# Kernel tuning notes

Hardware: AMD Instinct MI355X
Metric: run time of the kernel (lower is better)

## Reference

```python
import jax, jax.numpy as jnp
import numpy as np

B, NN, BBX, CLS, LAT = 8192, 64, 6, 16, 128
IN = LAT + NN + CLS  # 208
NT = B * NN          # total nodes in batched graph
NE = 4_194_304       # random edges (avg degree 8)


def setup_inputs() -> dict:
    key = jax.random.key(0)
    ks = jax.random.split(key, 16)
    p = lambda i, sh: (jax.random.normal(ks[i], sh, dtype=jnp.float32) * 0.05)
    return {
        "embedding": jax.random.normal(ks[0], (B, IN), dtype=jnp.float32),
        "E": jax.random.randint(ks[1], (2, NE), 0, NT, dtype=jnp.int32),
        "refine_iter": 2,
        "W1": p(2, (IN, 128)), "b1": p(3, (128,)),
        "W2": p(4, (128, 128)), "b2": p(5, (128,)),
        "Wbbx": p(6, (128, NN * BBX)), "bbbx": p(7, (NN * BBX,)),
        "Wlbl": p(8, (128, NN)), "blbl": p(9, (NN,)),
        "Wedge": p(10, (128, NN * NN)), "bedge": p(11, (NN * NN,)),
        "Wcls": p(12, (128, CLS)), "bcls": p(13, (CLS,)),
        "Wg": p(14, (BBX, BBX)), "bg": p(15, (BBX,)),
    }


def _gcn(h, src, dst, Wg, bg):
    # PyG GCNConv with add_self_loops=True, bias: D^-1/2 (A+I) D^-1/2 (h W) + b
    deg = jax.ops.segment_sum(jnp.ones(src.shape, h.dtype), dst, num_segments=NT)
    dinv = jax.lax.rsqrt(deg)  # deg >= 1 thanks to self-loops
    norm = dinv[src] * dinv[dst]
    m = h @ Wg  # [NT, BBX]
    out = jax.ops.segment_sum(m[src] * norm[:, None], dst, num_segments=NT)
    return out + bg


def reference(embedding, E, refine_iter, W1, b1, W2, b2, Wbbx, bbbx,
              Wlbl, blbl, Wedge, bedge, Wcls, bcls, Wg, bg):
    sig = jax.nn.sigmoid
    x = sig(embedding @ W1 + b1)
    x = sig(x @ W2 + b2)
    x = sig(x @ W2 + b2)  # dense2 applied twice (shared weights), as in source
    x_bbx = sig(x @ Wbbx + bbbx).reshape(B, NN, BBX)
    x_lbl = sig(x @ Wlbl + blbl).reshape(B, NN, 1)
    x_edge = sig(x @ Wedge + bedge).reshape(B, NN, NN)
    class_pred = jax.nn.softmax(x @ Wcls + bcls, axis=-1)

    loops = jnp.arange(NT, dtype=E.dtype)
    src = jnp.concatenate([E[0], loops])
    dst = jnp.concatenate([E[1], loops])

    x_bbx_refined = x_bbx
    for _ in range(int(refine_iter)):
        x_masked = x_bbx_refined * x_lbl  # labels=None -> mask with x_lbl
        flat = x_masked.reshape(NT, BBX)
        corr = jax.nn.sigmoid(_gcn(flat, src, dst, Wg, bg))
        # NOTE: source adds correction to the MASKED features (faithful)
        x_bbx_refined = (flat + corr).reshape(B, NN, BBX)
    return (x_bbx, x_lbl, x_edge, class_pred, x_bbx_refined)
```

## Files before the change

### kernel.cpp

```cpp
#include <hip/hip_runtime.h>
#include <hip/hip_bf16.h>
#include <math.h>

#define B_      8192
#define IN_     208
#define INP_    224
#define H_      128
#define NN_     64
#define BBX_    6
#define CLS_    16
#define NT_     (B_*NN_)
#define NE_     4194304
#define NB_     256
#define BSH_    11
#define CH_     4096
#define CAP_    18432

typedef __attribute__((ext_vector_type(8))) short short8v;
typedef __attribute__((ext_vector_type(4))) float f32x4;
typedef __attribute__((ext_vector_type(2))) float f32x2;

__device__ __forceinline__ float sigmoidf_(float v){ return 1.0f/(1.0f+__expf(-v)); }
__device__ __forceinline__ unsigned f2bf_(float f){
  unsigned u = __float_as_uint(f);
  return (u + 0x7FFFu + ((u >> 16) & 1u)) >> 16;
}

#if defined(__has_builtin)
# if __has_builtin(__builtin_amdgcn_cvt_pk_fp8_f32) && __has_builtin(__builtin_amdgcn_cvt_pk_f32_fp8)
#  define HW_FP8 1
# endif
#endif
#ifndef HW_FP8
# define HW_FP8 0
#endif

#if !HW_FP8
__device__ __forceinline__ unsigned enc1_(float v){
  unsigned u = __float_as_uint(v);
  unsigned s = (u >> 31) << 7;
  unsigned a = u & 0x7FFFFFFFu;
  unsigned r8;
  if (a < 0x3D000000u) {
    int q = (int)rintf(__uint_as_float(a) * 512.0f);
    r8 = (unsigned)q;
  } else {
    unsigned r = a + 0x7FFFFu + ((a >> 20) & 1u);
    int eb = (int)(r >> 23) - 120;
    r8 = (eb > 15) ? 0x7Eu : (unsigned)((eb << 3) | ((r >> 20) & 7u));
  }
  return s | r8;
}
__device__ __forceinline__ float dec1_(unsigned b){
  unsigned m = b & 7u, e = (b >> 3) & 0xFu;
  float mag = e ? __uint_as_float(((e + 120u) << 23) | (m << 20))
               : (float)m * 0.001953125f;
  return (b & 0x80u) ? -mag : mag;
}
#endif

__device__ __forceinline__ uint2 enc6_(const float mm[6]){
  uint2 o;
#if HW_FP8
  int w0 = __builtin_amdgcn_cvt_pk_fp8_f32(mm[0], mm[1], 0, false);
  w0     = __builtin_amdgcn_cvt_pk_fp8_f32(mm[2], mm[3], w0, true);
  int w1 = __builtin_amdgcn_cvt_pk_fp8_f32(mm[4], mm[5], 0, false);
  o.x = (unsigned)w0; o.y = (unsigned)w1;
#else
  o.x = enc1_(mm[0]) | (enc1_(mm[1])<<8) | (enc1_(mm[2])<<16) | (enc1_(mm[3])<<24);
  o.y = enc1_(mm[4]) | (enc1_(mm[5])<<8);
#endif
  return o;
}
__device__ __forceinline__ void dec6_(uint2 w, float v[6]){
#if HW_FP8
  f32x2 a = __builtin_amdgcn_cvt_pk_f32_fp8(w.x, false);
  f32x2 b = __builtin_amdgcn_cvt_pk_f32_fp8(w.x, true);
  f32x2 c = __builtin_amdgcn_cvt_pk_f32_fp8(w.y, false);
  v[0]=a[0]; v[1]=a[1]; v[2]=b[0]; v[3]=b[1]; v[4]=c[0]; v[5]=c[1];
#else
  v[0]=dec1_(w.x & 255u); v[1]=dec1_((w.x>>8)&255u);
  v[2]=dec1_((w.x>>16)&255u); v[3]=dec1_(w.x>>24);
  v[4]=dec1_(w.y & 255u); v[5]=dec1_((w.y>>8)&255u);
#endif
}

__global__ __launch_bounds__(256) void gemm_bias_act(
    const float* __restrict__ A, const float* __restrict__ W,
    const float* __restrict__ bias, float* __restrict__ C,
    int M, int N, int K, int act)
{
  __shared__ float As[16][64];
  __shared__ float Bs[16][64];
  const int tid = threadIdx.x;
  const int bm = blockIdx.y * 64;
  const int bn = blockIdx.x * 64;
  const int tx = tid & 15;
  const int ty = tid >> 4;
  const int arow = tid >> 2;
  const int acol = (tid & 3) << 2;
  const int brow = tid >> 4;
  const int bcol = (tid & 15) << 2;

  float acc[4][4] = {};

  for (int k0 = 0; k0 < K; k0 += 16) {
    float4 av = *reinterpret_cast<const float4*>(A + (size_t)(bm + arow) * K + k0 + acol);
    float4 bv = *reinterpret_cast<const float4*>(W + (size_t)(k0 + brow) * N + bn + bcol);
    __syncthreads();
    As[acol+0][arow] = av.x; As[acol+1][arow] = av.y;
    As[acol+2][arow] = av.z; As[acol+3][arow] = av.w;
    *reinterpret_cast<float4*>(&Bs[brow][bcol]) = bv;
    __syncthreads();
    #pragma unroll
    for (int k = 0; k < 16; ++k) {
      float4 a = *reinterpret_cast<const float4*>(&As[k][ty << 2]);
      float4 b = *reinterpret_cast<const float4*>(&Bs[k][tx << 2]);
      float ar[4] = {a.x, a.y, a.z, a.w};
      float br[4] = {b.x, b.y, b.z, b.w};
      #pragma unroll
      for (int i = 0; i < 4; ++i)
        #pragma unroll
        for (int j = 0; j < 4; ++j)
          acc[i][j] = fmaf(ar[i], br[j], acc[i][j]);
    }
  }

  #pragma unroll
  for (int i = 0; i < 4; ++i) {
    const int row = bm + (ty << 2) + i;
    float4 o;
    float* op = &o.x;
    #pragma unroll
    for (int j = 0; j < 4; ++j) {
      float v = acc[i][j] + bias[bn + (tx << 2) + j];
      op[j] = act ? sigmoidf_(v) : v;
    }
    *reinterpret_cast<float4*>(C + (size_t)row * N + bn + (tx << 2)) = o;
  }
}

__global__ __launch_bounds__(256) void prep_k(
    const float* __restrict__ We, unsigned short* __restrict__ WtE,
    const float* __restrict__ Wb, unsigned short* __restrict__ WtB,
    const float* __restrict__ W2, unsigned short* __restrict__ Wt2,
    const float* __restrict__ W1, unsigned short* __restrict__ W1t)
{
  __shared__ unsigned short tile[64][136];
  const int t = threadIdx.x;
  if (blockIdx.x >= 72) {
    const int i = (blockIdx.x - 72) * 256 + t;
    if (i < H_ * INP_) {
      const int n = i / INP_, k = i % INP_;
      W1t[i] = (k < IN_) ? (unsigned short)f2bf_(W1[(size_t)k * H_ + n]) : 0;
    }
    return;
  }
  const float* W; unsigned short* Wt; int N, n0;
  if (blockIdx.x < 64)      { W = We; Wt = WtE; N = 4096; n0 = blockIdx.x * 64; }
  else if (blockIdx.x < 70) { W = Wb; Wt = WtB; N = 384;  n0 = (blockIdx.x-64) * 64; }
  else                      { W = W2; Wt = Wt2; N = 128;  n0 = (blockIdx.x-70) * 64; }
  const int kk = t >> 6;
  const int nn = t & 63;
  for (int k0 = 0; k0 < 128; k0 += 4)
    tile[nn][k0 + kk] = (unsigned short)f2bf_(W[(size_t)(k0 + kk) * N + n0 + nn]);
  __syncthreads();
  const int rr = t >> 2, c0 = (t & 3) * 32;
  ushort4* dst = reinterpret_cast<ushort4*>(Wt + (size_t)(n0 + rr) * 128 + c0);
  #pragma unroll
  for (int q = 0; q < 8; ++q) {
    ushort4 o;
    o.x = tile[rr][c0 + q*4 + 0]; o.y = tile[rr][c0 + q*4 + 1];
    o.z = tile[rr][c0 + q*4 + 2]; o.w = tile[rr][c0 + q*4 + 3];
    dst[q] = o;
  }
}

__global__ __launch_bounds__(256) void fused_trunk_k(
    const float* __restrict__ emb,
    const unsigned short* __restrict__ W1t,
    const float* __restrict__ b1,
    const unsigned short* __restrict__ W2t,
    const float* __restrict__ b2,
    unsigned short* __restrict__ Xb, float* __restrict__ xB)
{
  __shared__ unsigned short s[128][136];
  const int tid  = threadIdx.x;
  const int wave = tid >> 6, lane = tid & 63;
  const int wm = wave >> 1, wn = wave & 1;
  const int r = lane & 15, g = lane >> 4;
  const int colB0 = wn * 64;
  const int growA = blockIdx.x * 128 + wm * 64;

  f32x4 acc[4][4];
  short8v a[4], b[4];

  #pragma unroll
  for (int i = 0; i < 4; ++i)
    #pragma unroll
    for (int j = 0; j < 4; ++j)
      acc[i][j] = (f32x4){0.f, 0.f, 0.f, 0.f};

  for (int ks = 0; ks < INP_/32; ++ks) {
    const int koff = ks * 32 + g * 8;
    #pragma unroll
    for (int i = 0; i < 4; ++i) {
      if (koff < IN_) {
        const float* src = emb + (size_t)(growA + i*16 + r) * IN_ + koff;
        float4 v0 = *reinterpret_cast<const float4*>(src);
        float4 v1 = *reinterpret_cast<const float4*>(src + 4);
        a[i][0]=(short)f2bf_(v0.x); a[i][1]=(short)f2bf_(v0.y);
        a[i][2]=(short)f2bf_(v0.z); a[i][3]=(short)f2bf_(v0.w);
        a[i][4]=(short)f2bf_(v1.x); a[i][5]=(short)f2bf_(v1.y);
        a[i][6]=(short)f2bf_(v1.z); a[i][7]=(short)f2bf_(v1.w);
      } else {
        a[i] = (short8v){0,0,0,0,0,0,0,0};
      }
    }
    #pragma unroll
    for (int j = 0; j < 4; ++j)
      b[j] = *reinterpret_cast<const short8v*>(W1t + (size_t)(colB0 + j*16 + r) * INP_ + koff);
    #pragma unroll
    for (int i = 0; i < 4; ++i)
      #pragma unroll
      for (int j = 0; j < 4; ++j)
        acc[i][j] = __builtin_amdgcn_mfma_f32_16x16x32_bf16(a[i], b[j], acc[i][j], 0, 0, 0);
  }
  #pragma unroll
  for (int j = 0; j < 4; ++j) {
    const int col = colB0 + j*16 + r;
    const float bc = b1[col];
    #pragma unroll
    for (int i = 0; i < 4; ++i)
      #pragma unroll
      for (int q = 0; q < 4; ++q)
        s[wm*64 + i*16 + g*4 + q][col] = (unsigned short)f2bf_(sigmoidf_(acc[i][j][q] + bc));
  }
  __syncthreads();

  for (int layer = 0; layer < 2; ++layer) {
    #pragma unroll
    for (int i = 0; i < 4; ++i)
      #pragma unroll
      for (int j = 0; j < 4; ++j)
        acc[i][j] = (f32x4){0.f, 0.f, 0.f, 0.f};

    #pragma unroll
    for (int ks = 0; ks < 4; ++ks) {
      const int koff = ks * 32 + g * 8;
      #pragma unroll
      for (int i = 0; i < 4; ++i)
        a[i] = *reinterpret_cast<const short8v*>(&s[wm*64 + i*16 + r][koff]);
      #pragma unroll
      for (int j = 0; j < 4; ++j)
        b[j] = *reinterpret_cast<const short8v*>(W2t + (size_t)(colB0 + j*16 + r) * H_ + koff);
      #pragma unroll
      for (int i = 0; i < 4; ++i)
        #pragma unroll
        for (int j = 0; j < 4; ++j)
          acc[i][j] = __builtin_amdgcn_mfma_f32_16x16x32_bf16(a[i], b[j], acc[i][j], 0, 0, 0);
    }
    __syncthreads();

    if (layer == 0) {
      #pragma unroll
      for (int j = 0; j < 4; ++j) {
        const int col = colB0 + j*16 + r;
        const float bc = b2[col];
        #pragma unroll
        for (int i = 0; i < 4; ++i)
          #pragma unroll
          for (int q = 0; q < 4; ++q)
            s[wm*64 + i*16 + g*4 + q][col] = (unsigned short)f2bf_(sigmoidf_(acc[i][j][q] + bc));
      }
      __syncthreads();
    } else {
      #pragma unroll
      for (int j = 0; j < 4; ++j) {
        const int col = colB0 + j*16 + r;
        const float bc = b2[col];
        #pragma unroll
        for (int i = 0; i < 4; ++i) {
          const int grow = blockIdx.x*128 + wm*64 + i*16 + g*4;
          #pragma unroll
          for (int q = 0; q < 4; ++q) {
            const float v = sigmoidf_(acc[i][j][q] + bc);
            Xb[(size_t)(grow + q) * H_ + col] = (unsigned short)f2bf_(v);
            xB[(size_t)(grow + q) * H_ + col] = v;
          }
        }
      }
    }
  }
}

__global__ __launch_bounds__(256) void gemm_mfma_head(
    const unsigned short* __restrict__ Xb,
    const unsigned short* __restrict__ Wt,
    const float* __restrict__ bias, float* __restrict__ C, int N)
{
  const int tid  = threadIdx.x;
  const int wave = tid >> 6, lane = tid & 63;
  const int wm = wave >> 1, wn = wave & 1;
  const int r = lane & 15, g = lane >> 4;
  const int rowA0 = blockIdx.y * 128 + wm * 64;
  const int colB0 = blockIdx.x * 128 + wn * 64;

  f32x4 acc[4][4];
  #pragma unroll
  for (int i = 0; i < 4; ++i)
    #pragma unroll
    for (int j = 0; j < 4; ++j)
      acc[i][j] = (f32x4){0.f, 0.f, 0.f, 0.f};

  #pragma unroll
  for (int ks = 0; ks < 4; ++ks) {
    const int koff = ks * 32 + g * 8;
    short8v a[4], b[4];
    #pragma unroll
    for (int i = 0; i < 4; ++i)
      a[i] = *reinterpret_cast<const short8v*>(Xb + (size_t)(rowA0 + i*16 + r) * 128 + koff);
    #pragma unroll
    for (int j = 0; j < 4; ++j)
      b[j] = *reinterpret_cast<const short8v*>(Wt + (size_t)(colB0 + j*16 + r) * 128 + koff);
    #pragma unroll
    for (int i = 0; i < 4; ++i)
      #pragma unroll
      for (int j = 0; j < 4; ++j)
        acc[i][j] = __builtin_amdgcn_mfma_f32_16x16x32_bf16(a[i], b[j], acc[i][j], 0, 0, 0);
  }

  #pragma unroll
  for (int j = 0; j < 4; ++j) {
    const int col = colB0 + j*16 + r;
    const float bc = bias[col];
    #pragma unroll
    for (int i = 0; i < 4; ++i) {
      const int row0 = rowA0 + i*16 + g*4;
      #pragma unroll
      for (int q = 0; q < 4; ++q)
        C[(size_t)(row0 + q) * N + col] = sigmoidf_(acc[i][j][q] + bc);
    }
  }
}

__global__ __launch_bounds__(64) void cls_softmax_k(
    const float* __restrict__ X, const float* __restrict__ Wc,
    const float* __restrict__ bc, float* __restrict__ out)
{
  const int tid = threadIdx.x;
  const int r = blockIdx.x * 4 + (tid >> 4);
  const int c = tid & 15;
  const float* xr = X + (size_t)r * H_;
  float acc = bc[c];
  #pragma unroll 8
  for (int k = 0; k < H_; ++k) acc = fmaf(xr[k], Wc[k * CLS_ + c], acc);
  float mx = acc;
  for (int off = 8; off; off >>= 1) mx = fmaxf(mx, __shfl_xor(mx, off, 16));
  float e = __expf(acc - mx);
  float s = e;
  for (int off = 8; off; off >>= 1) s += __shfl_xor(s, off, 16);
  out[(size_t)r * CLS_ + c] = e / s;
}

__global__ __launch_bounds__(256) void binA_k(const int* __restrict__ E,
                                              int* __restrict__ gcnt,
                                              unsigned* __restrict__ binned) {
  __shared__ unsigned stage[CH_];
  __shared__ unsigned char stb[CH_];
  __shared__ int hist[NB_], lbase[NB_], gbase[NB_];
  const int t = threadIdx.x;
  const int e0 = blockIdx.x * CH_;

  hist[t] = 0;
  __syncthreads();

  unsigned pk[CH_/256];
  int rb[CH_/256];
  #pragma unroll
  for (int i = 0; i < CH_/256; ++i) {
    const int e = e0 + i * 256 + t;
    const int s = E[e];
    const unsigned d = (unsigned)E[NE_ + e];
    const int b = d >> BSH_;
    pk[i] = (unsigned)s | ((d & 2047u) << 19);
    rb[i] = atomicAdd(&hist[b], 1) | (b << 20);
  }
  __syncthreads();

  const int v = hist[t];
  lbase[t] = v; __syncthreads();
  #pragma unroll
  for (int off = 1; off < NB_; off <<= 1) {
    int x = (t >= off) ? lbase[t - off] : 0;
    __syncthreads();
    lbase[t] += x;
    __syncthreads();
  }
  const int excl = lbase[t] - v;
  __syncthreads();
  lbase[t] = excl;
  gbase[t] = t * CAP_ + atomicAdd(&gcnt[t], v);
  __syncthreads();

  #pragma unroll
  for (int i = 0; i < CH_/256; ++i) {
    const int b = rb[i] >> 20;
    const int pos = lbase[b] + (rb[i] & 0xFFFFF);
    stage[pos] = pk[i];
    stb[pos] = (unsigned char)b;
  }
  __syncthreads();

  for (int i = t; i < CH_; i += 256) {
    const int b = stb[i];
    const int tgt = gbase[b] + (i - lbase[b]);
    if (tgt < (b + 1) * CAP_)
      binned[tgt] = stage[i];
  }
}

__global__ __launch_bounds__(1024) void csr_k(const int* __restrict__ gcnt,
                                              const unsigned* __restrict__ binned,
                                              int* __restrict__ rowptr, int* __restrict__ cnt_g,
                                              float* __restrict__ dinv, int* __restrict__ csr_src) {
  __shared__ int cnt[2048];
  __shared__ int sd[1024];
  const int t = threadIdx.x, b = blockIdx.x;
  const int beg = b * CAP_;
  const int end = beg + min(gcnt[b], CAP_);

  cnt[t] = 0; cnt[t + 1024] = 0;
  __syncthreads();
  for (int i = beg + t; i < end; i += 1024)
    atomicAdd(&cnt[binned[i] >> 19], 1);
  __syncthreads();

  const int c0 = cnt[2 * t], c1 = cnt[2 * t + 1];
  const int s = c0 + c1;
  sd[t] = s; __syncthreads();
  #pragma unroll
  for (int off = 1; off < 1024; off <<= 1) {
    int x = (t >= off) ? sd[t - off] : 0;
    __syncthreads();
    sd[t] += x;
    __syncthreads();
  }
  const int excl = sd[t] - s;

  const int node0 = b * 2048 + 2 * t;
  rowptr[node0]     = beg + excl;
  rowptr[node0 + 1] = beg + excl + c0;
  cnt_g[node0]      = c0;
  cnt_g[node0 + 1]  = c1;
  dinv[node0]       = rsqrtf(1.0f + (float)c0);
  dinv[node0 + 1]   = rsqrtf(1.0f + (float)c1);
  __syncthreads();
  cnt[2 * t] = excl;
  cnt[2 * t + 1] = excl + c0;
  __syncthreads();

  for (int i = beg + t; i < end; i += 1024) {
    const unsigned pk = binned[i];
    const int dl = pk >> 19;
    const int slot = atomicAdd(&cnt[dl], 1);
    csr_src[beg + slot] = (int)(pk & 0x7FFFFu);
  }
}

__global__ __launch_bounds__(256) void gcn_pre_k(
    const float* __restrict__ refined, const float* __restrict__ lbl,
    const float* __restrict__ Wg, const float* __restrict__ dinv,
    uint2* __restrict__ ms8)
{
  int i = blockIdx.x * 256 + threadIdx.x;
  if (i >= NT_) return;
  float l = lbl[i];
  float di = dinv[i];
  float f[6];
  #pragma unroll
  for (int j = 0; j < 6; ++j) f[j] = refined[(size_t)i * 6 + j] * l;
  float mm[6];
  #pragma unroll
  for (int j = 0; j < 6; ++j) {
    float acc = 0.f;
    #pragma unroll
    for (int k = 0; k < 6; ++k) acc = fmaf(f[k], Wg[k * 6 + j], acc);
    mm[j] = acc * di;
  }
  ms8[i] = enc6_(mm);
}

template<int WRITE_MS>
__global__ __launch_bounds__(256) void gcn_gather_k(
    const float* __restrict__ rin, float* __restrict__ rout,
    const float* __restrict__ lbl,
    const uint2* __restrict__ ms8_in, uint2* __restrict__ ms8_out,
    const float* __restrict__ dinv,
    const int* __restrict__ rowptr, const int* __restrict__ cnt,
    const int* __restrict__ csr_src, const float* __restrict__ bg,
    const float* __restrict__ Wg)
{
  int i = blockIdx.x * 256 + threadIdx.x;
  if (i >= NT_) return;
  const float di = dinv[i];
  const float l  = lbl[i];
  const int beg = rowptr[i];
  const int kend = beg + cnt[i];

  float acc[6];
  dec6_(ms8_in[i], acc);

  int k = beg;
  for (; k + 7 < kend; k += 8) {
    int s_[8];
    uint2 w_[8];
    #pragma unroll
    for (int u = 0; u < 8; ++u) s_[u] = csr_src[k + u];
    #pragma unroll
    for (int u = 0; u < 8; ++u) w_[u] = ms8_in[s_[u]];
    #pragma unroll
    for (int u = 0; u < 8; ++u) {
      float v[6];
      dec6_(w_[u], v);
      #pragma unroll
      for (int j = 0; j < 6; ++j) acc[j] += v[j];
    }
  }
  for (; k + 3 < kend; k += 4) {
    const int s0 = csr_src[k],   s1 = csr_src[k+1];
    const int s2 = csr_src[k+2], s3 = csr_src[k+3];
    const uint2 w0 = ms8_in[s0], w1 = ms8_in[s1];
    const uint2 w2 = ms8_in[s2], w3 = ms8_in[s3];
    float v0[6], v1[6], v2[6], v3[6];
    dec6_(w0, v0); dec6_(w1, v1); dec6_(w2, v2); dec6_(w3, v3);
    #pragma unroll
    for (int j = 0; j < 6; ++j) acc[j] += (v0[j] + v1[j]) + (v2[j] + v3[j]);
  }
  for (; k < kend; ++k) {
    float v[6];
    dec6_(ms8_in[csr_src[k]], v);
    #pragma unroll
    for (int j = 0; j < 6; ++j) acc[j] += v[j];
  }

  float nr[6];
  #pragma unroll
  for (int j = 0; j < 6; ++j) {
    const float flat = rin[(size_t)i * 6 + j] * l;
    nr[j] = flat + sigmoidf_(di * acc[j] + bg[j]);
    rout[(size_t)i * 6 + j] = nr[j];
  }

  if (WRITE_MS) {
    float f[6], mm[6];
    #pragma unroll
    for (int j = 0; j < 6; ++j) f[j] = nr[j] * l;
    #pragma unroll
    for (int j = 0; j < 6; ++j) {
      float a = 0.f;
      #pragma unroll
      for (int kk = 0; kk < 6; ++kk) a = fmaf(f[kk], Wg[kk * 6 + j], a);
      mm[j] = a * di;
    }
    ms8_out[i] = enc6_(mm);
  }
}

extern "C" void kernel_launch(void* const* d_in, const int* in_sizes, int n_in,
                              void* d_out, int out_size, void* d_ws, size_t ws_size,
                              hipStream_t stream)
{
  const float* emb   = (const float*)d_in[0];
  const int*   E     = (const int*)  d_in[1];
  const float* W1    = (const float*)d_in[3];
  const float* b1    = (const float*)d_in[4];
  const float* W2    = (const float*)d_in[5];
  const float* b2    = (const float*)d_in[6];
  const float* Wbbx  = (const float*)d_in[7];
  const float* bbbx  = (const float*)d_in[8];
  const float* Wlbl  = (const float*)d_in[9];
  const float* blbl  = (const float*)d_in[10];
  const float* Wedge = (const float*)d_in[11];
  const float* bedge = (const float*)d_in[12];
  const float* Wcls  = (const float*)d_in[13];
  const float* bcls  = (const float*)d_in[14];
  const float* Wg    = (const float*)d_in[15];
  const float* bg    = (const float*)d_in[16];

  float* out    = (float*)d_out;
  float* o_bbx  = out;
  float* o_lbl  = out + 3145728;
  float* o_edge = out + 3670016;
  float* o_cls  = out + 37224448;
  float* o_ref  = out + 37355520;

  char* wsb = (char*)d_ws;
  float* xB      = (float*)wsb;
  float* dinv    = xB + (size_t)B_ * H_;
  int*   cnt_g   = (int*)(dinv + NT_);
  int*   rowptr  = cnt_g + NT_;
  int*   csr_src = rowptr + NT_;
  char*  U       = (char*)(csr_src + (size_t)NB_ * CAP_);
  unsigned*       binned = (unsigned*)U;
  unsigned short* Xb   = (unsigned short*)U;
  unsigned short* W1t  = Xb  + (size_t)B_ * H_;
  unsigned short* W2t  = W1t + (size_t)H_ * INP_;
  unsigned short* Wt_e = W2t + (size_t)H_ * H_;
  unsigned short* Wt_b = Wt_e + (size_t)4096 * H_;
  uint2*          ms8A = (uint2*)(Wt_b + (size_t)384 * H_);
  uint2*          ms8B = ms8A + NT_;
  int*            gcnt = (int*)(U + (size_t)NB_ * CAP_ * 4);

  hipMemsetAsync(gcnt, 0, NB_ * sizeof(int), stream);
  binA_k<<<NE_/CH_, 256, 0, stream>>>(E, gcnt, binned);
  csr_k <<<NB_, 1024, 0, stream>>>(gcnt, binned, rowptr, cnt_g, dinv, csr_src);

  prep_k<<<72 + (H_*INP_+255)/256, 256, 0, stream>>>(Wedge, Wt_e, Wbbx, Wt_b, W2, W2t, W1, W1t);

  fused_trunk_k<<<B_/128, 256, 0, stream>>>(emb, W1t, b1, W2t, b2, Xb, xB);

  gemm_mfma_head<<<dim3(4096/128, B_/128), 256, 0, stream>>>(Xb, Wt_e, bedge, o_edge, 4096);
  gemm_mfma_head<<<dim3(384/128,  B_/128), 256, 0, stream>>>(Xb, Wt_b, bbbx,  o_bbx,  384);
  gemm_bias_act<<<dim3(64/64, B_/64), 256, 0, stream>>>(xB, Wlbl, blbl, o_lbl, B_, 64, 128, 1);
  cls_softmax_k<<<B_/4, 64, 0, stream>>>(xB, Wcls, bcls, o_cls);

  gcn_pre_k<<<NT_/256, 256, 0, stream>>>(o_bbx, o_lbl, Wg, dinv, ms8A);
  gcn_gather_k<1><<<NT_/256, 256, 0, stream>>>(o_bbx, o_ref, o_lbl, ms8A, ms8B,
                                               dinv, rowptr, cnt_g, csr_src, bg, Wg);
  gcn_gather_k<0><<<NT_/256, 256, 0, stream>>>(o_ref, o_ref, o_lbl, ms8B, nullptr,
                                               dinv, rowptr, cnt_g, csr_src, bg, Wg);
}
```

Before: 244.5 us.

## Fuse label and class-softmax heads into trunk kernel using MFMA

```diff
diff --git a/kernel.cpp b/kernel.cpp
--- a/kernel.cpp
+++ b/kernel.cpp
@@ -85,81 +85,33 @@
 #endif
 }
 
-__global__ __launch_bounds__(256) void gemm_bias_act(
-    const float* __restrict__ A, const float* __restrict__ W,
-    const float* __restrict__ bias, float* __restrict__ C,
-    int M, int N, int K, int act)
-{
-  __shared__ float As[16][64];
-  __shared__ float Bs[16][64];
-  const int tid = threadIdx.x;
-  const int bm = blockIdx.y * 64;
-  const int bn = blockIdx.x * 64;
-  const int tx = tid & 15;
-  const int ty = tid >> 4;
-  const int arow = tid >> 2;
-  const int acol = (tid & 3) << 2;
-  const int brow = tid >> 4;
-  const int bcol = (tid & 15) << 2;
-
-  float acc[4][4] = {};
-
-  for (int k0 = 0; k0 < K; k0 += 16) {
-    float4 av = *reinterpret_cast<const float4*>(A + (size_t)(bm + arow) * K + k0 + acol);
-    float4 bv = *reinterpret_cast<const float4*>(W + (size_t)(k0 + brow) * N + bn + bcol);
-    __syncthreads();
-    As[acol+0][arow] = av.x; As[acol+1][arow] = av.y;
-    As[acol+2][arow] = av.z; As[acol+3][arow] = av.w;
-    *reinterpret_cast<float4*>(&Bs[brow][bcol]) = bv;
-    __syncthreads();
-    #pragma unroll
-    for (int k = 0; k < 16; ++k) {
-      float4 a = *reinterpret_cast<const float4*>(&As[k][ty << 2]);
-      float4 b = *reinterpret_cast<const float4*>(&Bs[k][tx << 2]);
-      float ar[4] = {a.x, a.y, a.z, a.w};
-      float br[4] = {b.x, b.y, b.z, b.w};
-      #pragma unroll
-      for (int i = 0; i < 4; ++i)
-        #pragma unroll
-        for (int j = 0; j < 4; ++j)
-          acc[i][j] = fmaf(ar[i], br[j], acc[i][j]);
-    }
-  }
-
-  #pragma unroll
-  for (int i = 0; i < 4; ++i) {
-    const int row = bm + (ty << 2) + i;
-    float4 o;
-    float* op = &o.x;
-    #pragma unroll
-    for (int j = 0; j < 4; ++j) {
-      float v = acc[i][j] + bias[bn + (tx << 2) + j];
-      op[j] = act ? sigmoidf_(v) : v;
-    }
-    *reinterpret_cast<float4*>(C + (size_t)row * N + bn + (tx << 2)) = o;
-  }
-}
-
 __global__ __launch_bounds__(256) void prep_k(
     const float* __restrict__ We, unsigned short* __restrict__ WtE,
     const float* __restrict__ Wb, unsigned short* __restrict__ WtB,
     const float* __restrict__ W2, unsigned short* __restrict__ Wt2,
-    const float* __restrict__ W1, unsigned short* __restrict__ W1t)
+    const float* __restrict__ Wl, unsigned short* __restrict__ WtL,
+    const float* __restrict__ W1, unsigned short* __restrict__ W1t,
+    const float* __restrict__ Wc, unsigned short* __restrict__ WtC)
 {
   __shared__ unsigned short tile[64][136];
   const int t = threadIdx.x;
-  if (blockIdx.x >= 72) {
-    const int i = (blockIdx.x - 72) * 256 + t;
+  if (blockIdx.x >= 73) {
+    const int i = (blockIdx.x - 73) * 256 + t;
     if (i < H_ * INP_) {
       const int n = i / INP_, k = i % INP_;
       W1t[i] = (k < IN_) ? (unsigned short)f2bf_(W1[(size_t)k * H_ + n]) : 0;
+    } else if (i < H_ * INP_ + CLS_ * H_) {
+      const int j = i - H_ * INP_;
+      const int n = j >> 7, k = j & 127;
+      WtC[j] = (unsigned short)f2bf_(Wc[(size_t)k * CLS_ + n]);
     }
     return;
   }
   const float* W; unsigned short* Wt; int N, n0;
   if (blockIdx.x < 64)      { W = We; Wt = WtE; N = 4096; n0 = blockIdx.x * 64; }
   else if (blockIdx.x < 70) { W = Wb; Wt = WtB; N = 384;  n0 = (blockIdx.x-64) * 64; }
-  else                      { W = W2; Wt = Wt2; N = 128;  n0 = (blockIdx.x-70) * 64; }
+  else if (blockIdx.x < 72) { W = W2; Wt = Wt2; N = 128;  n0 = (blockIdx.x-70) * 64; }
+  else                      { W = Wl; Wt = WtL; N = 64;   n0 = 0; }
   const int kk = t >> 6;
   const int nn = t & 63;
   for (int k0 = 0; k0 < 128; k0 += 4)
@@ -182,21 +134,26 @@
     const float* __restrict__ b1,
     const unsigned short* __restrict__ W2t,
     const float* __restrict__ b2,
-    unsigned short* __restrict__ Xb, float* __restrict__ xB)
+    const unsigned short* __restrict__ WtL,
+    const float* __restrict__ blbl,
+    const unsigned short* __restrict__ WtC,
+    const float* __restrict__ bcls,
+    unsigned short* __restrict__ Xb,
+    float* __restrict__ o_lbl, float* __restrict__ o_cls)
 {
-  __shared__ unsigned short s[128][136];
+  __shared__ unsigned short s[64][136];
   const int tid  = threadIdx.x;
   const int wave = tid >> 6, lane = tid & 63;
   const int wm = wave >> 1, wn = wave & 1;
   const int r = lane & 15, g = lane >> 4;
   const int colB0 = wn * 64;
-  const int growA = blockIdx.x * 128 + wm * 64;
-
-  f32x4 acc[4][4];
-  short8v a[4], b[4];
-
-  #pragma unroll
-  for (int i = 0; i < 4; ++i)
+  const int grow0 = blockIdx.x * 64;
+
+  f32x4 acc[2][4];
+  short8v a[2], b[4];
+
+  #pragma unroll
+  for (int i = 0; i < 2; ++i)
     #pragma unroll
     for (int j = 0; j < 4; ++j)
       acc[i][j] = (f32x4){0.f, 0.f, 0.f, 0.f};
@@ -204,9 +161,9 @@
   for (int ks = 0; ks < INP_/32; ++ks) {
     const int koff = ks * 32 + g * 8;
     #pragma unroll
-    for (int i = 0; i < 4; ++i) {
+    for (int i = 0; i < 2; ++i) {
       if (koff < IN_) {
-        const float* src = emb + (size_t)(growA + i*16 + r) * IN_ + koff;
+        const float* src = emb + (size_t)(grow0 + wm*32 + i*16 + r) * IN_ + koff;
         float4 v0 = *reinterpret_cast<const float4*>(src);
         float4 v1 = *reinterpret_cast<const float4*>(src + 4);
         a[i][0]=(short)f2bf_(v0.x); a[i][1]=(short)f2bf_(v0.y);
@@ -221,7 +178,7 @@
     for (int j = 0; j < 4; ++j)
       b[j] = *reinterpret_cast<const short8v*>(W1t + (size_t)(colB0 + j*16 + r) * INP_ + koff);
     #pragma unroll
-    for (int i = 0; i < 4; ++i)
+    for (int i = 0; i < 2; ++i)
       #pragma unroll
       for (int j = 0; j < 4; ++j)
         acc[i][j] = __builtin_amdgcn_mfma_f32_16x16x32_bf16(a[i], b[j], acc[i][j], 0, 0, 0);
@@ -231,16 +188,16 @@
     const int col = colB0 + j*16 + r;
     const float bc = b1[col];
     #pragma unroll
-    for (int i = 0; i < 4; ++i)
+    for (int i = 0; i < 2; ++i)
       #pragma unroll
       for (int q = 0; q < 4; ++q)
-        s[wm*64 + i*16 + g*4 + q][col] = (unsigned short)f2bf_(sigmoidf_(acc[i][j][q] + bc));
+        s[wm*32 + i*16 + g*4 + q][col] = (unsigned short)f2bf_(sigmoidf_(acc[i][j][q] + bc));
   }
   __syncthreads();
 
   for (int layer = 0; layer < 2; ++layer) {
     #pragma unroll
-    for (int i = 0; i < 4; ++i)
+    for (int i = 0; i < 2; ++i)
       #pragma unroll
       for (int j = 0; j < 4; ++j)
         acc[i][j] = (f32x4){0.f, 0.f, 0.f, 0.f};
@@ -249,47 +206,84 @@
     for (int ks = 0; ks < 4; ++ks) {
       const int koff = ks * 32 + g * 8;
       #pragma unroll
-      for (int i = 0; i < 4; ++i)
-        a[i] = *reinterpret_cast<const short8v*>(&s[wm*64 + i*16 + r][koff]);
+      for (int i = 0; i < 2; ++i)
+        a[i] = *reinterpret_cast<const short8v*>(&s[wm*32 + i*16 + r][koff]);
       #pragma unroll
       for (int j = 0; j < 4; ++j)
         b[j] = *reinterpret_cast<const short8v*>(W2t + (size_t)(colB0 + j*16 + r) * H_ + koff);
       #pragma unroll
-      for (int i = 0; i < 4; ++i)
+      for (int i = 0; i < 2; ++i)
         #pragma unroll
         for (int j = 0; j < 4; ++j)
           acc[i][j] = __builtin_amdgcn_mfma_f32_16x16x32_bf16(a[i], b[j], acc[i][j], 0, 0, 0);
     }
     __syncthreads();
 
-    if (layer == 0) {
-      #pragma unroll
-      for (int j = 0; j < 4; ++j) {
-        const int col = colB0 + j*16 + r;
-        const float bc = b2[col];
+    #pragma unroll
+    for (int j = 0; j < 4; ++j) {
+      const int col = colB0 + j*16 + r;
+      const float bc = b2[col];
+      #pragma unroll
+      for (int i = 0; i < 2; ++i) {
         #pragma unroll
-        for (int i = 0; i < 4; ++i)
-          #pragma unroll
-          for (int q = 0; q < 4; ++q)
-            s[wm*64 + i*16 + g*4 + q][col] = (unsigned short)f2bf_(sigmoidf_(acc[i][j][q] + bc));
-      }
-      __syncthreads();
-    } else {
-      #pragma unroll
-      for (int j = 0; j < 4; ++j) {
-        const int col = colB0 + j*16 + r;
-        const float bc = b2[col];
-        #pragma unroll
-        for (int i = 0; i < 4; ++i) {
-          const int grow = blockIdx.x*128 + wm*64 + i*16 + g*4;
-          #pragma unroll
-          for (int q = 0; q < 4; ++q) {
-            const float v = sigmoidf_(acc[i][j][q] + bc);
-            Xb[(size_t)(grow + q) * H_ + col] = (unsigned short)f2bf_(v);
-            xB[(size_t)(grow + q) * H_ + col] = v;
-          }
+        for (int q = 0; q < 4; ++q) {
+          const float v = sigmoidf_(acc[i][j][q] + bc);
+          const unsigned short vb = (unsigned short)f2bf_(v);
+          s[wm*32 + i*16 + g*4 + q][col] = vb;
+          if (layer == 1)
+            Xb[(size_t)(grow0 + wm*32 + i*16 + g*4 + q) * H_ + col] = vb;
         }
       }
+    }
+    __syncthreads();
+  }
+
+  {
+    f32x4 accl[4];
+    #pragma unroll
+    for (int j = 0; j < 4; ++j) accl[j] = (f32x4){0.f, 0.f, 0.f, 0.f};
+    #pragma unroll
+    for (int ks = 0; ks < 4; ++ks) {
+      const int koff = ks * 32 + g * 8;
+      const short8v av = *reinterpret_cast<const short8v*>(&s[wave*16 + r][koff]);
+      #pragma unroll
+      for (int j = 0; j < 4; ++j) {
+        const short8v bv = *reinterpret_cast<const short8v*>(WtL + (size_t)(j*16 + r) * H_ + koff);
+        accl[j] = __builtin_amdgcn_mfma_f32_16x16x32_bf16(av, bv, accl[j], 0, 0, 0);
+      }
+    }
+    #pragma unroll
+    for (int j = 0; j < 4; ++j) {
+      const int col = j*16 + r;
+      const float bc = blbl[col];
+      #pragma unroll
+      for (int q = 0; q < 4; ++q) {
+        const int row = grow0 + wave*16 + g*4 + q;
+        o_lbl[(size_t)row * NN_ + col] = sigmoidf_(accl[j][q] + bc);
+      }
+    }
+  }
+
+  {
+    f32x4 accc = (f32x4){0.f, 0.f, 0.f, 0.f};
+    #pragma unroll
+    for (int ks = 0; ks < 4; ++ks) {
+      const int koff = ks * 32 + g * 8;
+      const short8v av = *reinterpret_cast<const short8v*>(&s[wave*16 + r][koff]);
+      const short8v bv = *reinterpret_cast<const short8v*>(WtC + (size_t)r * H_ + koff);
+      accc = __builtin_amdgcn_mfma_f32_16x16x32_bf16(av, bv, accc, 0, 0, 0);
+    }
+    const float bc = bcls[r];
+    #pragma unroll
+    for (int q = 0; q < 4; ++q) {
+      float v = accc[q] + bc;
+      float mx = v;
+      for (int off = 8; off; off >>= 1) mx = fmaxf(mx, __shfl_xor(mx, off, 16));
+      const float e = __expf(v - mx);
+      float sm = e;
+      for (int off = 8; off; off >>= 1) sm += __shfl_xor(sm, off, 16);
+      const int row = grow0 + wave*16 + g*4 + q;
+      o_cls[(size_t)row * CLS_ + r] = e / sm;
     }
   }
 }
@@ -342,25 +336,6 @@
         C[(size_t)(row0 + q) * N + col] = sigmoidf_(acc[i][j][q] + bc);
     }
   }
-}
-
-__global__ __launch_bounds__(64) void cls_softmax_k(
-    const float* __restrict__ X, const float* __restrict__ Wc,
-    const float* __restrict__ bc, float* __restrict__ out)
-{
-  const int tid = threadIdx.x;
-  const int r = blockIdx.x * 4 + (tid >> 4);
-  const int c = tid & 15;
-  const float* xr = X + (size_t)r * H_;
-  float acc = bc[c];
-  #pragma unroll 8
-  for (int k = 0; k < H_; ++k) acc = fmaf(xr[k], Wc[k * CLS_ + c], acc);
-  float mx = acc;
-  for (int off = 8; off; off >>= 1) mx = fmaxf(mx, __shfl_xor(mx, off, 16));
-  float e = __expf(acc - mx);
-  float s = e;
-  for (int off = 8; off; off >>= 1) s += __shfl_xor(s, off, 16);
-  out[(size_t)r * CLS_ + c] = e / s;
 }
 
 __global__ __launch_bounds__(256) void binA_k(const int* __restrict__ E,
@@ -596,8 +571,9 @@
   float* o_ref  = out + 37355520;
 
   char* wsb = (char*)d_ws;
-  float* xB      = (float*)wsb;
-  float* dinv    = xB + (size_t)B_ * H_;
+  unsigned short* WtL  = (unsigned short*)wsb;
+  unsigned short* WtC  = WtL + (size_t)NN_ * H_;
+  float* dinv    = (float*)(wsb + (size_t)1024 * 1024);
   int*   cnt_g   = (int*)(dinv + NT_);
   int*   rowptr  = cnt_g + NT_;
   int*   csr_src = rowptr + NT_;
@@ -616,14 +592,14 @@
   binA_k<<<NE_/CH_, 256, 0, stream>>>(E, gcnt, binned);
   csr_k <<<NB_, 1024, 0, stream>>>(gcnt, binned, rowptr, cnt_g, dinv, csr_src);
 
-  prep_k<<<72 + (H_*INP_+255)/256, 256, 0, stream>>>(Wedge, Wt_e, Wbbx, Wt_b, W2, W2t, W1, W1t);
-
-  fused_trunk_k<<<B_/128, 256, 0, stream>>>(emb, W1t, b1, W2t, b2, Xb, xB);
+  prep_k<<<73 + (H_*INP_ + CLS_*H_ + 255)/256, 256, 0, stream>>>(
+      Wedge, Wt_e, Wbbx, Wt_b, W2, W2t, Wlbl, WtL, W1, W1t, Wcls, WtC);
+
+  fused_trunk_k<<<B_/64, 256, 0, stream>>>(emb, W1t, b1, W2t, b2,
+                                           WtL, blbl, WtC, bcls, Xb, o_lbl, o_cls);
 
   gemm_mfma_head<<<dim3(4096/128, B_/128), 256, 0, stream>>>(Xb, Wt_e, bedge, o_edge, 4096);
   gemm_mfma_head<<<dim3(384/128,  B_/128), 256, 0, stream>>>(Xb, Wt_b, bbbx,  o_bbx,  384);
-  gemm_bias_act<<<dim3(64/64, B_/64), 256, 0, stream>>>(xB, Wlbl, blbl, o_lbl, B_, 64, 128, 1);
-  cls_softmax_k<<<B_/4, 64, 0, stream>>>(xB, Wcls, bcls, o_cls);
 
   gcn_pre_k<<<NT_/256, 256, 0, stream>>>(o_bbx, o_lbl, Wg, dinv, ms8A);
   gcn_gather_k<1><<<NT_/256, 256, 0, stream>>>(o_bbx, o_ref, o_lbl, ms8A, ms8B,
```

New measurement: 219.7 us. -10.2%, faster.
